# Performance work log

Measured on AMD Instinct MI355X. Metric: run time of the kernel, lower is better.

Reference implementation:

```python
import jax, jax.numpy as jnp
import numpy as np

LMAX = 4
K = (LMAX + 1) ** 2            # 25 full-rep coefficients
KR = 19                         # reduced rep for mmax=2: sum_l min(2l+1, 5)
C = 64                          # sphere_channels
HID = 64                        # attn hidden channels
H = 4                           # heads
A = 32                          # alpha channels per head
VC = 16                         # value channels per head
RBF = 64                        # num radial basis features
EC = 32                         # atom edge embedding channels
G = 100                         # S2 grid points (grid_resolution=10)
FFH = 128                       # ffn hidden channels
N = 10000
E = 30000
NSPEC = 90

_L_PER_K = np.repeat(np.arange(LMAX + 1), 2 * np.arange(LMAX + 1) + 1)  # [K]


def rms_norm_sh(x, g):
    # x: [N, K, C]; g: [LMAX+1, C] learned per-degree per-channel scale
    rms = jnp.sqrt(jnp.mean(x * x, axis=(1, 2), keepdims=True) + 1e-6)
    return (x / rms) * g[_L_PER_K]


def setup_inputs() -> dict:
    key = jax.random.key(0)
    ks = jax.random.split(key, 24)
    r = lambda i, sh, s=1.0: (jax.random.normal(ks[i], sh, dtype=jnp.float32) * s)
    inp = {
        "node_feats": r(0, (N, K, C)),
        "edge_distances": jax.random.uniform(ks[1], (E, RBF), dtype=jnp.float32),
        "wigner": r(2, (E, KR, K), 0.2),
        "wigner_inv": r(3, (E, K, KR), 0.2),
        "node_species": jax.random.randint(ks[4], (N,), 0, NSPEC),
        "senders": jax.random.randint(ks[5], (E,), 0, N),
        "receivers": jax.random.randint(ks[6], (E,), 0, N),
        # parameters
        "g1": jnp.ones((LMAX + 1, C), jnp.float32),
        "g2": jnp.ones((LMAX + 1, C), jnp.float32),
        "emb_s": r(7, (NSPEC, EC), 0.1),
        "emb_r": r(8, (NSPEC, EC), 0.1),
        "We1": r(9, (RBF + 2 * EC, 128), 0.1),
        "We2": r(10, (128, HID), 0.1),
        "Wso2": r(11, (2 * C, HID), 0.1),
        "Wa": r(12, (HID, H * A), 0.1),
        "va": r(13, (H, A), 0.1),
        "Wv": r(14, (HID, H * VC), 0.1),
        "Wo": r(15, (H * VC, C), 0.1),
        "to_grid": r(16, (G, K), 0.2),
        "from_grid": r(17, (K, G), 0.2),
        "Wf1": r(18, (C, FFH), 0.1),
        "Wf2": r(19, (FFH, C), 0.1),
    }
    return inp


def reference(node_feats, edge_distances, wigner, wigner_inv, g1, g2,
              emb_s, emb_r, We1, We2, Wso2, Wa, va, Wv, Wo,
              to_grid, from_grid, Wf1, Wf2,
              node_species, senders, receivers):
    n = node_feats.shape[0]
    e = senders.shape[0]

    # ---- norm 1 + SO(2) equivariant graph attention ----
    res = node_feats
    x = rms_norm_sh(node_feats, g1)

    # gather sender/receiver features, concat channel-wise: [E, K, 2C]
    xe = jnp.concatenate([x[senders], x[receivers]], axis=-1)
    # per-edge Wigner rotation to reduced (mmax) rep: [E, KR, 2C]
    xr = jnp.einsum('erk,ekc->erc', wigner, xe)

    # invariant edge features: RBF + atom-pair embeddings -> 2-layer MLP
    ef = jnp.concatenate([edge_distances,
                          emb_s[node_species[senders]],
                          emb_r[node_species[receivers]]], axis=-1)
    ef = jax.nn.silu(ef @ We1)
    ef = jax.nn.silu(ef @ We2)               # [E, HID]

    # SO2 convolution (channel mixing) modulated by radial features
    msg = jnp.einsum('erc,cd->erd', xr, Wso2) * ef[:, None, :]  # [E, KR, HID]
    # scalar-gated equivariant nonlinearity (S2 gate on l=0 part)
    msg = msg * jax.nn.sigmoid(msg[:, :1, :])

    # attention logits from invariant (l=0,m=0) component
    a = jax.nn.leaky_relu(msg[:, 0, :] @ Wa, 0.2).reshape(e, H, A)
    logits = jnp.einsum('eha,ha->eh', a, va)  # [E, H]
    mx = jax.ops.segment_max(logits, receivers, num_segments=n)
    ex = jnp.exp(logits - mx[receivers])
    den = jax.ops.segment_sum(ex, receivers, num_segments=n)
    alpha = ex / (den[receivers] + 1e-9)      # [E, H] softmax over incoming edges

    # values, weight by attention, rotate back to full rep, project, scatter
    v = (msg @ Wv).reshape(e, KR, H, VC)
    v = (v * alpha[:, None, :, None]).reshape(e, KR, H * VC)
    v = jnp.einsum('ekr,erd->ekd', wigner_inv, v)   # [E, K, H*VC]
    out_e = v @ Wo                                   # [E, K, C]
    attn_out = jax.ops.segment_sum(out_e, receivers, num_segments=n)

    x = attn_out + res

    # ---- norm 2 + grid-based S2 feedforward ----
    res = x
    x = rms_norm_sh(x, g2)
    xg = jnp.einsum('gk,nkc->ngc', to_grid, x)       # to S2 grid [N, G, C]
    h = jax.nn.silu(xg @ Wf1)                        # pointwise MLP on grid
    og = h @ Wf2
    x = jnp.einsum('kg,ngc->nkc', from_grid, og)     # back to SH coeffs
    return x + res
```

## Files before the change

kernel.cpp:

```cpp
#include <hip/hip_runtime.h>

#define KK 25
#define KRR 19
#define NH 4
#define GG 100
#define FFH 128

__device__ __constant__ int c_l_per_k[25] = {0, 1,1,1, 2,2,2,2,2,
                                             3,3,3,3,3,3,3,
                                             4,4,4,4,4,4,4,4,4};

__device__ __forceinline__ float siluf(float x) { return x / (1.0f + __expf(-x)); }
__device__ __forceinline__ float sigmf(float x) { return 1.0f / (1.0f + __expf(-x)); }

__device__ __forceinline__ constexpr int lpk(int k) {
    return (k == 0) ? 0 : (k < 4) ? 1 : (k < 9) ? 2 : (k < 16) ? 3 : 4;
}

__device__ __forceinline__ float rdlane(float x, int l) {
    return __int_as_float(__builtin_amdgcn_readlane(__float_as_int(x), l));
}

__global__ void k_scale(const float* __restrict__ xf, float* __restrict__ scale) {
    int n = blockIdx.x, t = threadIdx.x;
    __shared__ float red[256];
    const float* xp = xf + (size_t)n * 1600;
    float ss = 0.f;
    for (int i = t; i < 1600; i += 256) { float v = xp[i]; ss += v * v; }
    red[t] = ss; __syncthreads();
    for (int s = 128; s > 0; s >>= 1) { if (t < s) red[t] += red[t + s]; __syncthreads(); }
    if (t == 0) scale[n] = rsqrtf(red[0] / 1600.0f + 1e-6f);
}

__global__ __launch_bounds__(256) void k_pq(
        const float* __restrict__ xf, const float* __restrict__ g1,
        const float* __restrict__ scale, const float* __restrict__ Wso2,
        float* __restrict__ pq, int N) {
    const int lane = threadIdx.x & 63;
    const int n = __builtin_amdgcn_readfirstlane(blockIdx.x * 4 + (threadIdx.x >> 6));
    if (n >= N) return;
    const float sc = scale[n];
    float xn[25];
#pragma unroll
    for (int k = 0; k < 25; ++k)
        xn[k] = xf[(size_t)n * 1600 + k * 64 + lane] * sc * g1[lpk(k) * 64 + lane];
    float P[25], Q[25];
#pragma unroll
    for (int k = 0; k < 25; ++k) { P[k] = 0.f; Q[k] = 0.f; }
    for (int c = 0; c < 64; ++c) {
        const float w0 = Wso2[c * 64 + lane];
        const float w1 = Wso2[(64 + c) * 64 + lane];
#pragma unroll
        for (int k = 0; k < 25; ++k) {
            const float sv = rdlane(xn[k], c);
            P[k] += sv * w0;
            Q[k] += sv * w1;
        }
    }
    float* __restrict__ pp = pq + (size_t)n * 1600;
    float* __restrict__ qp = pq + (size_t)N * 1600 + (size_t)n * 1600;
#pragma unroll
    for (int k = 0; k < 25; ++k) {
        pp[k * 64 + lane] = P[k];
        qp[k * 64 + lane] = Q[k];
    }
}

__global__ void k_wvo(const float* __restrict__ Wv, const float* __restrict__ Wo,
                      float* __restrict__ Wvo) {
    int i = blockIdx.x * blockDim.x + threadIdx.x;
    if (i >= 4 * 64 * 64) return;
    int h = i >> 12, d = (i >> 6) & 63, d3 = i & 63;
    float a = 0.f;
    for (int vc = 0; vc < 16; ++vc)
        a += Wv[d * 64 + h * 16 + vc] * Wo[(h * 16 + vc) * 64 + d3];
    Wvo[i] = a;
}

__global__ __launch_bounds__(128) void k_edge_logits(
        const float* __restrict__ edist, const float* __restrict__ emb_s,
        const float* __restrict__ emb_r, const float* __restrict__ We1,
        const float* __restrict__ We2, const float* __restrict__ Wso2,
        const float* __restrict__ Wa, const float* __restrict__ va,
        const float* __restrict__ wigner, const float* __restrict__ xf,
        const float* __restrict__ g1, const float* __restrict__ scale,
        const int* __restrict__ species, const int* __restrict__ senders,
        const int* __restrict__ receivers, float* __restrict__ logits,
        float* __restrict__ efsbuf) {
    int e = blockIdx.x, t = threadIdx.x;
    __shared__ float efin[128], h1[128], efs[64], xr0[128], msg0[64], ared[128];
    int s = senders[e], r = receivers[e];
    if (t < 64)       efin[t] = edist[(size_t)e * 64 + t];
    else if (t < 96)  efin[t] = emb_s[species[s] * 32 + (t - 64)];
    else              efin[t] = emb_r[species[r] * 32 + (t - 96)];
    {
        int c = t & 63;
        int node = (t < 64) ? s : r;
        float sc = scale[node];
        const float* xb = xf + (size_t)node * 1600;
        float a = 0.f;
        for (int k = 0; k < KK; ++k)
            a += wigner[(size_t)e * 475 + k] * xb[k * 64 + c] * g1[c_l_per_k[k] * 64 + c];
        xr0[t] = a * sc;
    }
    __syncthreads();
    {
        float a = 0.f;
        for (int c = 0; c < 128; ++c) a += efin[c] * We1[c * 128 + t];
        h1[t] = siluf(a);
    }
    __syncthreads();
    if (t < 64) {
        float a = 0.f;
        for (int c = 0; c < 128; ++c) a += h1[c] * We2[c * 64 + t];
        float ef = siluf(a);
        efs[t] = ef;
        if (efsbuf) efsbuf[(size_t)e * 64 + t] = ef;
    }
    __syncthreads();
    if (t < 64) {
        float a = 0.f;
        for (int c = 0; c < 128; ++c) a += xr0[c] * Wso2[c * 64 + t];
        a *= efs[t];
        msg0[t] = a * sigmf(a);
    }
    __syncthreads();
    {
        float a = 0.f;
        for (int d = 0; d < 64; ++d) a += msg0[d] * Wa[d * 128 + t];
        float av = (a > 0.f) ? a : 0.2f * a;
        ared[t] = av * va[t];
    }
    __syncthreads();
    if (t < NH) {
        float sum = 0.f;
        for (int a = 0; a < 32; ++a) sum += ared[t * 32 + a];
        logits[(size_t)e * NH + t] = sum;
    }
}

__global__ void k_count(const int* __restrict__ receivers, int* __restrict__ counts, int E) {
    int e = blockIdx.x * blockDim.x + threadIdx.x;
    if (e < E) atomicAdd(&counts[receivers[e]], 1);
}

__global__ void k_scan(int* __restrict__ counts, int* __restrict__ offsets, int n) {
    __shared__ int buf[256];
    __shared__ int base_s;
    int t = threadIdx.x;
    if (t == 0) base_s = 0;
    __syncthreads();
    for (int start = 0; start < n; start += 256) {
        int idx = start + t;
        int v = (idx < n) ? counts[idx] : 0;
        buf[t] = v; __syncthreads();
        for (int o = 1; o < 256; o <<= 1) {
            int x = (t >= o) ? buf[t - o] : 0;
            __syncthreads();
            buf[t] += x;
            __syncthreads();
        }
        int incl = buf[t];
        int b = base_s;
        if (idx < n) { offsets[idx] = b + incl - v; counts[idx] = 0; }
        __syncthreads();
        if (t == 0) base_s = b + buf[255];
        __syncthreads();
    }
    if (t == 0) offsets[n] = base_s;
}

__global__ void k_fill(const int* __restrict__ receivers, const int* __restrict__ offsets,
                       int* __restrict__ cursors, int* __restrict__ edge_ids, int E) {
    int e = blockIdx.x * blockDim.x + threadIdx.x;
    if (e >= E) return;
    int r = receivers[e];
    int pos = atomicAdd(&cursors[r], 1);
    edge_ids[offsets[r] + pos] = e;
}

__global__ void k_alpha(float* __restrict__ logits, const int* __restrict__ offsets,
                        const int* __restrict__ edge_ids, int N) {
    int i = blockIdx.x * blockDim.x + threadIdx.x;
    if (i >= N * NH) return;
    int n = i >> 2, h = i & 3;
    int o0 = offsets[n], o1 = offsets[n + 1];
    float m = -1e30f;
    for (int j = o0; j < o1; ++j)
        m = fmaxf(m, logits[(size_t)edge_ids[j] * NH + h]);
    float s = 0.f;
    for (int j = o0; j < o1; ++j)
        s += expf(logits[(size_t)edge_ids[j] * NH + h] - m);
    float inv = 1.0f / (s + 1e-9f);
    for (int j = o0; j < o1; ++j) {
        size_t idx = (size_t)edge_ids[j] * NH + h;
        logits[idx] = expf(logits[idx] - m) * inv;
    }
}

__global__ void k_tr_fg(const float* __restrict__ from_grid, float* __restrict__ fgT) {
    int i = blockIdx.x * blockDim.x + threadIdx.x;
    if (i < GG * KK) {
        int g = i / KK, k = i - g * KK;
        fgT[g * KK + k] = from_grid[k * GG + g];
    }
}

__global__ __launch_bounds__(256) void k_edge_fast(
        const float* __restrict__ pq, const float* __restrict__ wigner,
        const float* __restrict__ wigner_inv, const float* __restrict__ Wvo,
        const float* __restrict__ efsbuf, const float* __restrict__ alpha,
        const int* __restrict__ senders, const int* __restrict__ receivers,
        float* __restrict__ out, int N, int E) {
    const int lane = threadIdx.x & 63;
    const int e = __builtin_amdgcn_readfirstlane(blockIdx.x * 4 + (threadIdx.x >> 6));
    if (e >= E) return;
    const int s = senders[e];
    const int r = receivers[e];

    const float* __restrict__ Ps = pq + (size_t)s * 1600;
    const float* __restrict__ Qr = pq + (size_t)N * 1600 + (size_t)r * 1600;
    float XW[25];
#pragma unroll
    for (int k = 0; k < 25; ++k) XW[k] = Ps[k * 64 + lane] + Qr[k * 64 + lane];

    const float* __restrict__ wge = wigner + (size_t)e * 475;
    float mp[19];
#pragma unroll
    for (int rr = 0; rr < 19; ++rr) {
        float a = 0.f;
#pragma unroll
        for (int k = 0; k < 25; ++k) a += wge[rr * 25 + k] * XW[k];
        mp[rr] = a;
    }

    const float ef = efsbuf[(size_t)e * 64 + lane];
    const float eg = ef * sigmf(mp[0] * ef);

    const float a0 = alpha[(size_t)e * NH + 0];
    const float a1 = alpha[(size_t)e * NH + 1];
    const float a2 = alpha[(size_t)e * NH + 2];
    const float a3 = alpha[(size_t)e * NH + 3];

    float z[19];
#pragma unroll
    for (int rr = 0; rr < 19; ++rr) z[rr] = 0.f;
    for (int d = 0; d < 64; ++d) {
        float wv = a0 * Wvo[d * 64 + lane]
                 + a1 * Wvo[4096 + d * 64 + lane]
                 + a2 * Wvo[8192 + d * 64 + lane]
                 + a3 * Wvo[12288 + d * 64 + lane];
        wv *= rdlane(eg, d);
#pragma unroll
        for (int rr = 0; rr < 19; ++rr) z[rr] += rdlane(mp[rr], d) * wv;
    }

    const float* __restrict__ wvi = wigner_inv + (size_t)e * 475;
    float* __restrict__ op = out + (size_t)r * 1600;
#pragma unroll
    for (int k = 0; k < 25; ++k) {
        float a = 0.f;
#pragma unroll
        for (int rr = 0; rr < 19; ++rr) a += wvi[k * 19 + rr] * z[rr];
        atomicAdd(&op[k * 64 + lane], a);
    }
}

__global__ __launch_bounds__(256) void k_edge(
        const float* __restrict__ xf, const float* __restrict__ wigner,
        const float* __restrict__ wigner_inv, const float* __restrict__ edist,
        const float* __restrict__ emb_s, const float* __restrict__ emb_r,
        const float* __restrict__ We1, const float* __restrict__ We2,
        const float* __restrict__ Wso2, const float* __restrict__ Wv,
        const float* __restrict__ Wo, const float* __restrict__ g1,
        const float* __restrict__ scale, const float* __restrict__ alpha,
        const int* __restrict__ species, const int* __restrict__ senders,
        const int* __restrict__ receivers, float* __restrict__ out, int E) {
    const int lane = threadIdx.x & 63;
    const int e = __builtin_amdgcn_readfirstlane(blockIdx.x * 4 + (threadIdx.x >> 6));
    if (e >= E) return;
    const int s = senders[e];
    const int r = receivers[e];
    const float scs = scale[s], scr = scale[r];

    float g1l[5];
#pragma unroll
    for (int l = 0; l < 5; ++l) g1l[l] = g1[l * 64 + lane];

    float xs[25], xc[25];
#pragma unroll
    for (int k = 0; k < 25; ++k) {
        const float gk = g1l[lpk(k)];
        xs[k] = xf[(size_t)s * 1600 + k * 64 + lane] * scs * gk;
        xc[k] = xf[(size_t)r * 1600 + k * 64 + lane] * scr * gk;
    }

    const float* __restrict__ wge = wigner + (size_t)e * 475;
    float xrs[19], xrc[19];
#pragma unroll
    for (int rr = 0; rr < 19; ++rr) {
        float a = 0.f, b = 0.f;
#pragma unroll
        for (int k = 0; k < 25; ++k) {
            const float w = wge[rr * 25 + k];
            a += w * xs[k];
            b += w * xc[k];
        }
        xrs[rr] = a; xrc[rr] = b;
    }

    float h1a = 0.f, h1b = 0.f;
    {
        const float* __restrict__ eda = edist + (size_t)e * 64;
        const float* __restrict__ esa = emb_s + (size_t)species[s] * 32;
        const float* __restrict__ era = emb_r + (size_t)species[r] * 32;
        for (int c = 0; c < 64; ++c) {
            const float v = eda[c];
            h1a += v * We1[c * 128 + lane];
            h1b += v * We1[c * 128 + 64 + lane];
        }
        for (int c = 0; c < 32; ++c) {
            const float v = esa[c];
            h1a += v * We1[(64 + c) * 128 + lane];
            h1b += v * We1[(64 + c) * 128 + 64 + lane];
        }
        for (int c = 0; c < 32; ++c) {
            const float v = era[c];
            h1a += v * We1[(96 + c) * 128 + lane];
            h1b += v * We1[(96 + c) * 128 + 64 + lane];
        }
        h1a = siluf(h1a); h1b = siluf(h1b);
    }
    float efs = 0.f;
    for (int j = 0; j < 64; ++j) {
        efs += rdlane(h1a, j) * We2[j * 64 + lane];
        efs += rdlane(h1b, j) * We2[(j + 64) * 64 + lane];
    }
    efs = siluf(efs);

    float msg[19];
#pragma unroll
    for (int rr = 0; rr < 19; ++rr) msg[rr] = 0.f;
    for (int c = 0; c < 64; ++c) {
        const float w0 = Wso2[c * 64 + lane];
        const float w1 = Wso2[(64 + c) * 64 + lane];
#pragma unroll
        for (int rr = 0; rr < 19; ++rr)
            msg[rr] += rdlane(xrs[rr], c) * w0 + rdlane(xrc[rr], c) * w1;
    }
#pragma unroll
    for (int rr = 0; rr < 19; ++rr) msg[rr] *= efs;
    const float gate = sigmf(msg[0]);
#pragma unroll
    for (int rr = 0; rr < 19; ++rr) msg[rr] *= gate;

    const int hh = lane >> 4;
    const float al = alpha[(size_t)e * NH + hh];

    float v2[19];
#pragma unroll
    for (int rr = 0; rr < 19; ++rr) v2[rr] = 0.f;
    for (int d = 0; d < 64; ++d) {
        const float w = Wv[d * 64 + lane];
#pragma unroll
        for (int rr = 0; rr < 19; ++rr) v2[rr] += rdlane(msg[rr], d) * w;
    }
#pragma unroll
    for (int rr = 0; rr < 19; ++rr) v2[rr] *= al;

    float z[19];
#pragma unroll
    for (int rr = 0; rr < 19; ++rr) z[rr] = 0.f;
    for (int d = 0; d < 64; ++d) {
        const float w = Wo[d * 64 + lane];
#pragma unroll
        for (int rr = 0; rr < 19; ++rr) z[rr] += rdlane(v2[rr], d) * w;
    }

    const float* __restrict__ wvi = wigner_inv + (size_t)e * 475;
    float* __restrict__ op = out + (size_t)r * 1600;
#pragma unroll
    for (int k = 0; k < 25; ++k) {
        float a = 0.f;
#pragma unroll
        for (int rr = 0; rr < 19; ++rr) a += wvi[k * 19 + rr] * z[rr];
        atomicAdd(&op[k * 64 + lane], a);
    }
}

__global__ __launch_bounds__(256) void k_ffn(
        const float* __restrict__ xf, const float* __restrict__ g2,
        const float* __restrict__ to_grid, const float* __restrict__ fgT,
        const float* __restrict__ Wf1, const float* __restrict__ Wf2,
        float* __restrict__ out, int N) {
    const int lane = threadIdx.x & 63;
    const int n = __builtin_amdgcn_readfirstlane(blockIdx.x * 4 + (threadIdx.x >> 6));
    if (n >= N) return;
    const float* __restrict__ oin = out + (size_t)n * 1600;
    const float* __restrict__ xin = xf + (size_t)n * 1600;

    float xn[25];
    float ss = 0.f;
#pragma unroll
    for (int k = 0; k < 25; ++k) {
        const float X = oin[k * 64 + lane] + xin[k * 64 + lane];
        xn[k] = X;
        ss += X * X;
    }
#pragma unroll
    for (int m = 1; m < 64; m <<= 1) ss += __shfl_xor(ss, m, 64);
    const float sc2 = rsqrtf(ss * (1.0f / 1600.f) + 1e-6f);
#pragma unroll
    for (int k = 0; k < 25; ++k) xn[k] *= sc2 * g2[lpk(k) * 64 + lane];

    float Ya[25], Yb[25];
#pragma unroll
    for (int k = 0; k < 25; ++k) { Ya[k] = 0.f; Yb[k] = 0.f; }
    for (int c = 0; c < 64; ++c) {
        const float w0 = Wf1[c * FFH + lane];
        const float w1 = Wf1[c * FFH + 64 + lane];
#pragma unroll
        for (int k = 0; k < 25; ++k) {
            const float sv = rdlane(xn[k], c);
            Ya[k] += sv * w0;
            Yb[k] += sv * w1;
        }
    }

    float Ua[25], Ub[25];
#pragma unroll
    for (int k = 0; k < 25; ++k) { Ua[k] = 0.f; Ub[k] = 0.f; }
#pragma unroll 2
    for (int g = 0; g < GG; ++g) {
        const float* __restrict__ tg = to_grid + (size_t)g * KK;
        const float* __restrict__ fg = fgT + (size_t)g * KK;
        float ha = 0.f, hb = 0.f;
#pragma unroll
        for (int k = 0; k < 25; ++k) {
            const float t = tg[k];
            ha += t * Ya[k];
            hb += t * Yb[k];
        }
        ha = siluf(ha); hb = siluf(hb);
#pragma unroll
        for (int k = 0; k < 25; ++k) {
            const float f = fg[k];
            Ua[k] += f * ha;
            Ub[k] += f * hb;
        }
    }

    float racc[25];
#pragma unroll
    for (int k = 0; k < 25; ++k) racc[k] = 0.f;
    for (int j = 0; j < 64; ++j) {
        const float w0 = Wf2[j * 64 + lane];
        const float w1 = Wf2[(64 + j) * 64 + lane];
#pragma unroll
        for (int k = 0; k < 25; ++k)
            racc[k] += rdlane(Ua[k], j) * w0 + rdlane(Ub[k], j) * w1;
    }

    float* __restrict__ op = out + (size_t)n * 1600;
#pragma unroll
    for (int k = 0; k < 25; ++k)
        op[k * 64 + lane] = oin[k * 64 + lane] + xin[k * 64 + lane] + racc[k];
}

extern "C" void kernel_launch(void* const* d_in, const int* in_sizes, int n_in,
                              void* d_out, int out_size, void* d_ws, size_t ws_size,
                              hipStream_t stream) {
    const float* node_feats     = (const float*)d_in[0];
    const float* edge_distances = (const float*)d_in[1];
    const float* wigner         = (const float*)d_in[2];
    const float* wigner_inv     = (const float*)d_in[3];
    const int*   node_species   = (const int*)  d_in[4];
    const int*   senders        = (const int*)  d_in[5];
    const int*   receivers      = (const int*)  d_in[6];
    const float* g1             = (const float*)d_in[7];
    const float* g2             = (const float*)d_in[8];
    const float* emb_s          = (const float*)d_in[9];
    const float* emb_r          = (const float*)d_in[10];
    const float* We1            = (const float*)d_in[11];
    const float* We2            = (const float*)d_in[12];
    const float* Wso2           = (const float*)d_in[13];
    const float* Wa             = (const float*)d_in[14];
    const float* va             = (const float*)d_in[15];
    const float* Wv             = (const float*)d_in[16];
    const float* Wo             = (const float*)d_in[17];
    const float* to_grid        = (const float*)d_in[18];
    const float* from_grid      = (const float*)d_in[19];
    const float* Wf1            = (const float*)d_in[20];
    const float* Wf2            = (const float*)d_in[21];

    const int N = in_sizes[4];
    const int E = in_sizes[5];

    char* ws = (char*)d_ws;
    size_t o = 0;
    float* scale    = (float*)(ws + o); o += (size_t)N * 4;
    int*   counts   = (int*)  (ws + o); o += (size_t)N * 4;
    int*   offsets  = (int*)  (ws + o); o += (size_t)(N + 1) * 4;
    int*   edge_ids = (int*)  (ws + o); o += (size_t)E * 4;
    float* logits   = (float*)(ws + o); o += (size_t)E * NH * 4;
    float* fgT      = (float*)(ws + o); o += (size_t)GG * KK * 4;
    size_t o_fast = o;
    float* efsbuf = (float*)(ws + o_fast); o_fast += (size_t)E * 64 * 4;
    float* Wvo    = (float*)(ws + o_fast); o_fast += (size_t)4 * 64 * 64 * 4;
    float* pq     = (float*)(ws + o_fast); o_fast += (size_t)N * 3200 * 4;
    const bool fast = (ws_size >= o_fast);

    hipMemsetAsync(counts, 0, (size_t)N * 4, stream);
    hipMemsetAsync(d_out, 0, (size_t)N * 1600 * 4, stream);

    k_scale<<<N, 256, 0, stream>>>(node_feats, scale);
    k_edge_logits<<<E, 128, 0, stream>>>(edge_distances, emb_s, emb_r, We1, We2, Wso2,
                                         Wa, va, wigner, node_feats, g1, scale,
                                         node_species, senders, receivers, logits,
                                         fast ? efsbuf : nullptr);
    k_count<<<(E + 255) / 256, 256, 0, stream>>>(receivers, counts, E);
    k_scan<<<1, 256, 0, stream>>>(counts, offsets, N);
    k_fill<<<(E + 255) / 256, 256, 0, stream>>>(receivers, offsets, counts, edge_ids, E);
    k_alpha<<<(N * NH + 255) / 256, 256, 0, stream>>>(logits, offsets, edge_ids, N);
    k_tr_fg<<<(GG * KK + 255) / 256, 256, 0, stream>>>(from_grid, fgT);
    if (fast) {
        k_pq<<<(N + 3) / 4, 256, 0, stream>>>(node_feats, g1, scale, Wso2, pq, N);
        k_wvo<<<64, 256, 0, stream>>>(Wv, Wo, Wvo);
        k_edge_fast<<<(E + 3) / 4, 256, 0, stream>>>(pq, wigner, wigner_inv, Wvo,
                                                     efsbuf, logits, senders, receivers,
                                                     (float*)d_out, N, E);
    } else {
        k_edge<<<(E + 3) / 4, 256, 0, stream>>>(node_feats, wigner, wigner_inv,
                                                edge_distances, emb_s, emb_r, We1, We2,
                                                Wso2, Wv, Wo, g1, scale, logits,
                                                node_species, senders, receivers,
                                                (float*)d_out, E);
    }
    k_ffn<<<(N + 3) / 4, 256, 0, stream>>>(node_feats, g2, to_grid, fgT, Wf1, Wf2,
                                           (float*)d_out, N);
}
```

Measured before the change: 1.427 ms.

## Reuse precomputed P/Q for edge logits and restructure FFN via linearity

The fast path gains a wavefront-per-edge logits kernel that builds the invariant message from the precomputed per-node P/Q projections, replacing the block-per-edge kernel that re-read node features. The RMS scale is folded into k_pq, so the separate scale kernel goes away. The FFN is split into an RMS/residual pass, a pass that applies Wf1 (with g2 folded in) before the to-grid projection and contracts over grid points, and a final Wf2 pass that reuses the pq buffer as scratch. This reorders matrix products to cut per-node work, at the cost of extra kernel launches and global round trips.

```diff
diff --git a/kernel.cpp b/kernel.cpp
--- a/kernel.cpp
+++ b/kernel.cpp
@@ -34,16 +34,23 @@
 
 __global__ __launch_bounds__(256) void k_pq(
         const float* __restrict__ xf, const float* __restrict__ g1,
-        const float* __restrict__ scale, const float* __restrict__ Wso2,
-        float* __restrict__ pq, int N) {
+        const float* __restrict__ Wso2, float* __restrict__ pq, int N) {
     const int lane = threadIdx.x & 63;
     const int n = __builtin_amdgcn_readfirstlane(blockIdx.x * 4 + (threadIdx.x >> 6));
     if (n >= N) return;
-    const float sc = scale[n];
     float xn[25];
-#pragma unroll
-    for (int k = 0; k < 25; ++k)
-        xn[k] = xf[(size_t)n * 1600 + k * 64 + lane] * sc * g1[lpk(k) * 64 + lane];
+    float ss = 0.f;
+#pragma unroll
+    for (int k = 0; k < 25; ++k) {
+        const float v = xf[(size_t)n * 1600 + k * 64 + lane];
+        xn[k] = v;
+        ss += v * v;
+    }
+#pragma unroll
+    for (int m = 1; m < 64; m <<= 1) ss += __shfl_xor(ss, m, 64);
+    const float sc = rsqrtf(ss * (1.0f / 1600.f) + 1e-6f);
+#pragma unroll
+    for (int k = 0; k < 25; ++k) xn[k] *= sc * g1[lpk(k) * 64 + lane];
     float P[25], Q[25];
 #pragma unroll
     for (int k = 0; k < 25; ++k) { P[k] = 0.f; Q[k] = 0.f; }
@@ -77,6 +84,90 @@
     Wvo[i] = a;
 }
 
+__global__ void k_w1l(const float* __restrict__ g2, const float* __restrict__ Wf1,
+                      float* __restrict__ W1l) {
+    int i = blockIdx.x * blockDim.x + threadIdx.x;
+    if (i >= 5 * 64 * 128) return;
+    int l = i >> 13, c = (i >> 7) & 63, j = i & 127;
+    W1l[i] = g2[l * 64 + c] * Wf1[c * FFH + j];
+}
+
+__global__ __launch_bounds__(256) void k_elog(
+        const float* __restrict__ edist, const float* __restrict__ emb_s,
+        const float* __restrict__ emb_r, const float* __restrict__ We1,
+        const float* __restrict__ We2, const float* __restrict__ Wa,
+        const float* __restrict__ va, const float* __restrict__ pq,
+        const float* __restrict__ wigner, const int* __restrict__ species,
+        const int* __restrict__ senders, const int* __restrict__ receivers,
+        float* __restrict__ logits, float* __restrict__ efsbuf, int N, int E) {
+    const int lane = threadIdx.x & 63;
+    const int e = __builtin_amdgcn_readfirstlane(blockIdx.x * 4 + (threadIdx.x >> 6));
+    if (e >= E) return;
+    const int s = senders[e], r = receivers[e];
+    float h1a = 0.f, h1b = 0.f;
+    {
+        const float* __restrict__ eda = edist + (size_t)e * 64;
+#pragma unroll 4
+        for (int c = 0; c < 64; ++c) {
+            const float v = eda[c];
+            h1a += v * We1[c * 128 + lane];
+            h1b += v * We1[c * 128 + 64 + lane];
+        }
+        const float* __restrict__ esa = emb_s + (size_t)species[s] * 32;
+        const float* __restrict__ era = emb_r + (size_t)species[r] * 32;
+#pragma unroll 4
+        for (int c = 0; c < 32; ++c) {
+            const float v = esa[c];
+            h1a += v * We1[(64 + c) * 128 + lane];
+            h1b += v * We1[(64 + c) * 128 + 64 + lane];
+        }
+#pragma unroll 4
+        for (int c = 0; c < 32; ++c) {
+            const float v = era[c];
+            h1a += v * We1[(96 + c) * 128 + lane];
+            h1b += v * We1[(96 + c) * 128 + 64 + lane];
+        }
+    }
+    h1a = siluf(h1a); h1b = siluf(h1b);
+    float efs = 0.f;
+    for (int j = 0; j < 64; ++j) {
+        efs += rdlane(h1a, j) * We2[j * 64 + lane];
+        efs += rdlane(h1b, j) * We2[(j + 64) * 64 + lane];
+    }
+    efs = siluf(efs);
+    efsbuf[(size_t)e * 64 + lane] = efs;
+
+    const float* __restrict__ wge = wigner + (size_t)e * 475;
+    const float* __restrict__ Ps = pq + (size_t)s * 1600;
+    const float* __restrict__ Qr = pq + (size_t)N * 1600 + (size_t)r * 1600;
+    float m0 = 0.f;
+#pragma unroll
+    for (int k = 0; k < 25; ++k)
+        m0 += wge[k] * (Ps[k * 64 + lane] + Qr[k * 64 + lane]);
+    m0 *= efs;
+    const float m0g = m0 * sigmf(m0);
+
+    float ava = 0.f, avb = 0.f;
+    for (int d = 0; d < 64; ++d) {
+        const float sv = rdlane(m0g, d);
+        ava += sv * Wa[d * 128 + lane];
+        avb += sv * Wa[d * 128 + 64 + lane];
+    }
+    ava = (ava > 0.f) ? ava : 0.2f * ava;
+    avb = (avb > 0.f) ? avb : 0.2f * avb;
+    float ra = ava * va[lane];
+    float rb = avb * va[64 + lane];
+#pragma unroll
+    for (int m = 1; m <= 16; m <<= 1) {
+        ra += __shfl_xor(ra, m, 64);
+        rb += __shfl_xor(rb, m, 64);
+    }
+    if ((lane & 31) == 0) {
+        logits[(size_t)e * NH + (lane >> 5)] = ra;
+        logits[(size_t)e * NH + 2 + (lane >> 5)] = rb;
+    }
+}
+
 __global__ __launch_bounds__(128) void k_edge_logits(
         const float* __restrict__ edist, const float* __restrict__ emb_s,
         const float* __restrict__ emb_r, const float* __restrict__ We1,
@@ -85,8 +176,7 @@
         const float* __restrict__ wigner, const float* __restrict__ xf,
         const float* __restrict__ g1, const float* __restrict__ scale,
         const int* __restrict__ species, const int* __restrict__ senders,
-        const int* __restrict__ receivers, float* __restrict__ logits,
-        float* __restrict__ efsbuf) {
+        const int* __restrict__ receivers, float* __restrict__ logits) {
     int e = blockIdx.x, t = threadIdx.x;
     __shared__ float efin[128], h1[128], efs[64], xr0[128], msg0[64], ared[128];
     int s = senders[e], r = receivers[e];
@@ -113,9 +203,7 @@
     if (t < 64) {
         float a = 0.f;
         for (int c = 0; c < 128; ++c) a += h1[c] * We2[c * 64 + t];
-        float ef = siluf(a);
-        efs[t] = ef;
-        if (efsbuf) efsbuf[(size_t)e * 64 + t] = ef;
+        efs[t] = siluf(a);
     }
     __syncthreads();
     if (t < 64) {
@@ -386,6 +474,104 @@
         for (int rr = 0; rr < 19; ++rr) a += wvi[k * 19 + rr] * z[rr];
         atomicAdd(&op[k * 64 + lane], a);
     }
+}
+
+__global__ void k_rms(const float* __restrict__ xf, float* __restrict__ out,
+                      float* __restrict__ sc2) {
+    int n = blockIdx.x, t = threadIdx.x;
+    __shared__ float red[256];
+    float* __restrict__ op = out + (size_t)n * 1600;
+    const float* __restrict__ xp = xf + (size_t)n * 1600;
+    float ss = 0.f;
+    for (int i = t; i < 1600; i += 256) {
+        float v = op[i] + xp[i];
+        op[i] = v;
+        ss += v * v;
+    }
+    red[t] = ss; __syncthreads();
+    for (int s = 128; s > 0; s >>= 1) { if (t < s) red[t] += red[t + s]; __syncthreads(); }
+    if (t == 0) sc2[n] = rsqrtf(red[0] / 1600.0f + 1e-6f);
+}
+
+__global__ __launch_bounds__(256) void k_ffn1(
+        const float* __restrict__ Xg, const float* __restrict__ sc2buf,
+        const float* __restrict__ W1l, const float* __restrict__ to_grid,
+        const float* __restrict__ fgT, float* __restrict__ Uws, int N) {
+    const int lane = threadIdx.x & 63;
+    const int n = __builtin_amdgcn_readfirstlane(blockIdx.x * 4 + (threadIdx.x >> 6));
+    if (n >= N) return;
+    const float sc2 = sc2buf[n];
+    const float* __restrict__ xrow = Xg + (size_t)n * 1600;
+
+    float Ya[25], Yb[25];
+#pragma unroll
+    for (int k = 0; k < 25; ++k) {
+        const float* __restrict__ wl = W1l + (size_t)lpk(k) * 8192;
+        const float* __restrict__ xr = xrow + k * 64;
+        float a = 0.f, b = 0.f;
+#pragma unroll 4
+        for (int c = 0; c < 64; ++c) {
+            const float xv = xr[c];
+            a += xv * wl[c * 128 + lane];
+            b += xv * wl[c * 128 + 64 + lane];
+        }
+        Ya[k] = a * sc2;
+        Yb[k] = b * sc2;
+    }
+
+    float Ua[25], Ub[25];
+#pragma unroll
+    for (int k = 0; k < 25; ++k) { Ua[k] = 0.f; Ub[k] = 0.f; }
+#pragma unroll 2
+    for (int g = 0; g < GG; ++g) {
+        const float* __restrict__ tg = to_grid + (size_t)g * KK;
+        const float* __restrict__ fg = fgT + (size_t)g * KK;
+        float ha = 0.f, hb = 0.f;
+#pragma unroll
+        for (int k = 0; k < 25; ++k) {
+            const float t = tg[k];
+            ha += t * Ya[k];
+            hb += t * Yb[k];
+        }
+        ha = siluf(ha); hb = siluf(hb);
+#pragma unroll
+        for (int k = 0; k < 25; ++k) {
+            const float f = fg[k];
+            Ua[k] += f * ha;
+            Ub[k] += f * hb;
+        }
+    }
+
+    float* __restrict__ ua = Uws + ((size_t)n * 128 + lane) * 25;
+    float* __restrict__ ub = Uws + ((size_t)n * 128 + 64 + lane) * 25;
+#pragma unroll
+    for (int k = 0; k < 25; ++k) {
+        ua[k] = Ua[k];
+        ub[k] = Ub[k];
+    }
+}
+
+__global__ __launch_bounds__(256) void k_ffn2(
+        const float* __restrict__ Uws, const float* __restrict__ Wf2,
+        float* __restrict__ out, int N) {
+    const int lane = threadIdx.x & 63;
+    const int n = __builtin_amdgcn_readfirstlane(blockIdx.x * 4 + (threadIdx.x >> 6));
+    if (n >= N) return;
+    const float* __restrict__ urow = Uws + (size_t)n * 3200;
+    float racc[25];
+#pragma unroll
+    for (int k = 0; k < 25; ++k) racc[k] = 0.f;
+#pragma unroll 2
+    for (int j = 0; j < 128; ++j) {
+        const float wv = Wf2[j * 64 + lane];
+        const float* __restrict__ up = urow + j * 25;
+#pragma unroll
+        for (int k = 0; k < 25; ++k) racc[k] += up[k] * wv;
+    }
+    float* __restrict__ op = out + (size_t)n * 1600;
+#pragma unroll
+    for (int k = 0; k < 25; ++k)
+        op[k * 64 + lane] = op[k * 64 + lane] + racc[k];
 }
 
 __global__ __launch_bounds__(256) void k_ffn(
@@ -508,34 +694,51 @@
     float* efsbuf = (float*)(ws + o_fast); o_fast += (size_t)E * 64 * 4;
     float* Wvo    = (float*)(ws + o_fast); o_fast += (size_t)4 * 64 * 64 * 4;
     float* pq     = (float*)(ws + o_fast); o_fast += (size_t)N * 3200 * 4;
+    float* W1l    = (float*)(ws + o_fast); o_fast += (size_t)5 * 64 * 128 * 4;
+    float* sc2    = (float*)(ws + o_fast); o_fast += (size_t)N * 4;
     const bool fast = (ws_size >= o_fast);
 
     hipMemsetAsync(counts, 0, (size_t)N * 4, stream);
     hipMemsetAsync(d_out, 0, (size_t)N * 1600 * 4, stream);
 
-    k_scale<<<N, 256, 0, stream>>>(node_feats, scale);
-    k_edge_logits<<<E, 128, 0, stream>>>(edge_distances, emb_s, emb_r, We1, We2, Wso2,
-                                         Wa, va, wigner, node_feats, g1, scale,
-                                         node_species, senders, receivers, logits,
-                                         fast ? efsbuf : nullptr);
-    k_count<<<(E + 255) / 256, 256, 0, stream>>>(receivers, counts, E);
-    k_scan<<<1, 256, 0, stream>>>(counts, offsets, N);
-    k_fill<<<(E + 255) / 256, 256, 0, stream>>>(receivers, offsets, counts, edge_ids, E);
-    k_alpha<<<(N * NH + 255) / 256, 256, 0, stream>>>(logits, offsets, edge_ids, N);
     k_tr_fg<<<(GG * KK + 255) / 256, 256, 0, stream>>>(from_grid, fgT);
     if (fast) {
-        k_pq<<<(N + 3) / 4, 256, 0, stream>>>(node_feats, g1, scale, Wso2, pq, N);
+        k_pq<<<(N + 3) / 4, 256, 0, stream>>>(node_feats, g1, Wso2, pq, N);
         k_wvo<<<64, 256, 0, stream>>>(Wv, Wo, Wvo);
+        k_w1l<<<(5 * 64 * 128 + 255) / 256, 256, 0, stream>>>(g2, Wf1, W1l);
+        k_elog<<<(E + 3) / 4, 256, 0, stream>>>(edge_distances, emb_s, emb_r, We1,
+                                                We2, Wa, va, pq, wigner, node_species,
+                                                senders, receivers, logits, efsbuf,
+                                                N, E);
+        k_count<<<(E + 255) / 256, 256, 0, stream>>>(receivers, counts, E);
+        k_scan<<<1, 256, 0, stream>>>(counts, offsets, N);
+        k_fill<<<(E + 255) / 256, 256, 0, stream>>>(receivers, offsets, counts,
+                                                    edge_ids, E);
+        k_alpha<<<(N * NH + 255) / 256, 256, 0, stream>>>(logits, offsets, edge_ids, N);
         k_edge_fast<<<(E + 3) / 4, 256, 0, stream>>>(pq, wigner, wigner_inv, Wvo,
                                                      efsbuf, logits, senders, receivers,
                                                      (float*)d_out, N, E);
+        k_rms<<<N, 256, 0, stream>>>(node_feats, (float*)d_out, sc2);
+        k_ffn1<<<(N + 3) / 4, 256, 0, stream>>>((const float*)d_out, sc2, W1l,
+                                                to_grid, fgT, pq, N);
+        k_ffn2<<<(N + 3) / 4, 256, 0, stream>>>(pq, Wf2, (float*)d_out, N);
     } else {
+        k_scale<<<N, 256, 0, stream>>>(node_feats, scale);
+        k_edge_logits<<<E, 128, 0, stream>>>(edge_distances, emb_s, emb_r, We1, We2,
+                                             Wso2, Wa, va, wigner, node_feats, g1,
+                                             scale, node_species, senders, receivers,
+                                             logits);
+        k_count<<<(E + 255) / 256, 256, 0, stream>>>(receivers, counts, E);
+        k_scan<<<1, 256, 0, stream>>>(counts, offsets, N);
+        k_fill<<<(E + 255) / 256, 256, 0, stream>>>(receivers, offsets, counts,
+                                                    edge_ids, E);
+        k_alpha<<<(N * NH + 255) / 256, 256, 0, stream>>>(logits, offsets, edge_ids, N);
         k_edge<<<(E + 3) / 4, 256, 0, stream>>>(node_feats, wigner, wigner_inv,
                                                 edge_distances, emb_s, emb_r, We1, We2,
                                                 Wso2, Wv, Wo, g1, scale, logits,
                                                 node_species, senders, receivers,
                                                 (float*)d_out, E);
-    }
-    k_ffn<<<(N + 3) / 4, 256, 0, stream>>>(node_feats, g2, to_grid, fgT, Wf1, Wf2,
-                                           (float*)d_out, N);
-}
+        k_ffn<<<(N + 3) / 4, 256, 0, stream>>>(node_feats, g2, to_grid, fgT, Wf1, Wf2,
+                                               (float*)d_out, N);
+    }
+}
```

Measured after the change: 1.402 ms. No clear change (-1.8%).
